# Optimization experiments

Measured on AMD Instinct MI355X. Metric: run time of the kernel, lower is better.

The kernel has to match this reference:

```python
import jax, jax.numpy as jnp
import numpy as np

K = 10  # knn neighbors
EPS = 1e-5  # BatchNorm eps


def mish(x):
    # x * tanh(softplus(x)), numerically stable softplus
    return x * jnp.tanh(jnp.logaddexp(x, 0.0))


def bn(x, g, b, m, v, nd):
    # inference-mode BatchNorm over channel axis 1
    shp = (1, -1) + (1,) * (nd - 2)
    scale = g.reshape(shp) / jnp.sqrt(v.reshape(shp) + EPS)
    return (x - m.reshape(shp)) * scale + b.reshape(shp)


def graph_feature(x, k):
    # x: [B, C, N] -> edge features [B, 2C, N, k]
    xt = jnp.swapaxes(x, 1, 2)  # [B, N, C]
    sq = jnp.sum(x * x, axis=1)  # [B, N]
    # negative squared pairwise distance [B, N, N]
    neg = 2.0 * jnp.einsum('bcn,bcm->bnm', x, x) - sq[:, :, None] - sq[:, None, :]
    idx = jax.lax.top_k(neg, k)[1]  # [B, N, k] nearest-neighbor indices
    nbr = jax.vmap(lambda a, i: a[i])(xt, idx)  # [B, N, k, C]
    ctr = jnp.broadcast_to(xt[:, :, None, :], nbr.shape)
    feat = jnp.concatenate([nbr - ctr, ctr], axis=-1)  # [B, N, k, 2C]
    return jnp.transpose(feat, (0, 3, 1, 2))  # [B, 2C, N, k]


def c2(w, x):  # 1x1 Conv2d
    return jnp.einsum('oc,bcnk->bonk', w, x)


def c1(w, x):  # 1x1 Conv1d
    return jnp.einsum('oc,bcn->bon', w, x)


def setup_inputs() -> dict:
    key = jax.random.key(0)
    ks = jax.random.split(key, 32)
    B, d, N = 8, 3, 2048
    emb, nb = 1024, 6
    def w(k_, o, c):
        return jax.random.normal(k_, (o, c), dtype=jnp.float32) * (1.0 / np.sqrt(c))
    inp = {
        'x': jax.random.normal(ks[0], (B, d, N), dtype=jnp.float32),
        'w1': w(ks[1], 64, 2 * d), 'w2': w(ks[2], 64, 64),
        'w3': w(ks[3], 64, 128), 'w4': w(ks[4], 64, 64),
        'w5': w(ks[5], 64, 128), 'w6': w(ks[6], emb, 192),
        'w7': w(ks[7], 512, emb + 192), 'w8': w(ks[8], 256, 512),
        'w9': w(ks[9], d * nb, 256),
        'g15': jax.random.uniform(ks[10], (5, 64), jnp.float32, 0.5, 1.5),
        'b15': jax.random.normal(ks[11], (5, 64), jnp.float32) * 0.1,
        'm15': jax.random.normal(ks[12], (5, 64), jnp.float32) * 0.1,
        'v15': jax.random.uniform(ks[13], (5, 64), jnp.float32, 0.5, 1.5),
        'g6': jax.random.uniform(ks[14], (emb,), jnp.float32, 0.5, 1.5),
        'b6': jax.random.normal(ks[15], (emb,), jnp.float32) * 0.1,
        'm6': jax.random.normal(ks[16], (emb,), jnp.float32) * 0.1,
        'v6': jax.random.uniform(ks[17], (emb,), jnp.float32, 0.5, 1.5),
        'g7': jax.random.uniform(ks[18], (512,), jnp.float32, 0.5, 1.5),
        'b7': jax.random.normal(ks[19], (512,), jnp.float32) * 0.1,
        'm7': jax.random.normal(ks[20], (512,), jnp.float32) * 0.1,
        'v7': jax.random.uniform(ks[21], (512,), jnp.float32, 0.5, 1.5),
        'g8': jax.random.uniform(ks[22], (256,), jnp.float32, 0.5, 1.5),
        'b8': jax.random.normal(ks[23], (256,), jnp.float32) * 0.1,
        'm8': jax.random.normal(ks[24], (256,), jnp.float32) * 0.1,
        'v8': jax.random.uniform(ks[25], (256,), jnp.float32, 0.5, 1.5),
    }
    return inp


def reference(x, w1, w2, w3, w4, w5, w6, w7, w8, w9,
              g15, b15, m15, v15, g6, b6, m6, v6,
              g7, b7, m7, v7, g8, b8, m8, v8):
    N = x.shape[2]
    f = graph_feature(x, K)                                   # [B, 6, N, K]
    h = mish(bn(c2(w1, f), g15[0], b15[0], m15[0], v15[0], 4))
    h = mish(bn(c2(w2, h), g15[1], b15[1], m15[1], v15[1], 4))
    x1 = jnp.max(h, axis=-1)                                  # [B, 64, N]
    f = graph_feature(x1, K)
    h = mish(bn(c2(w3, f), g15[2], b15[2], m15[2], v15[2], 4))
    h = mish(bn(c2(w4, h), g15[3], b15[3], m15[3], v15[3], 4))
    x2 = jnp.max(h, axis=-1)
    f = graph_feature(x2, K)
    h = mish(bn(c2(w5, f), g15[4], b15[4], m15[4], v15[4], 4))
    x3 = jnp.max(h, axis=-1)
    cat = jnp.concatenate([x1, x2, x3], axis=1)               # [B, 192, N]
    h6 = mish(bn(c1(w6, cat), g6, b6, m6, v6, 3))             # [B, emb, N]
    glob = jnp.max(h6, axis=-1, keepdims=True)
    glob = jnp.broadcast_to(glob, (glob.shape[0], glob.shape[1], N))
    h = jnp.concatenate([glob, cat], axis=1)                  # [B, emb+192, N]
    h = mish(bn(c1(w7, h), g7, b7, m7, v7, 3))
    h = mish(bn(c1(w8, h), g8, b8, m8, v8, 3))
    return c1(w9, h)                                          # [B, 18, N]
```

## Files before the change

kernel.cpp:

```cpp
#include <hip/hip_runtime.h>
#include <math.h>

#define BN_EPS 1e-5f
typedef unsigned long long u64;
typedef __attribute__((ext_vector_type(8))) short bf16x8;
typedef __attribute__((ext_vector_type(8))) unsigned short u16x8;
typedef __attribute__((ext_vector_type(4))) float f32x4;

__device__ __forceinline__ float mishf(float x){
  float u = __expf(fminf(x, 20.f));
  float w = u * (u + 2.f);
  return x * w / (w + 2.f);
}

__device__ __forceinline__ unsigned fenc(float f){
  unsigned u = __float_as_uint(f);
  return u ^ ((unsigned)((int)u >> 31) | 0x80000000u);
}
__device__ __forceinline__ float fdec(unsigned e){
  unsigned u = (e & 0x80000000u) ? (e & 0x7fffffffu) : ~e;
  return __uint_as_float(u);
}

__device__ __forceinline__ void bfsplit(float a, unsigned short &h, unsigned short &l){
  unsigned u = __float_as_uint(a);
  unsigned hb = (u + 0x7FFFu + ((u >> 16) & 1u)) >> 16;
  h = (unsigned short)hb;
  float hf = __uint_as_float(hb << 16);
  float r = a - hf;
  unsigned v = __float_as_uint(r);
  l = (unsigned short)((v + 0x7FFFu + ((v >> 16) & 1u)) >> 16);
}

__device__ __forceinline__ u64 mkkey(float v, int i){
  return ((u64)fenc(v) << 32) | (unsigned)(~i);
}
__device__ __forceinline__ int keyidx(u64 k){ return (int)(~(unsigned)k); }

__device__ __forceinline__ void ins10k(u64 (&L)[10], u64 k){
  if (k <= L[9]) return;
  #pragma unroll
  for (int p = 9; p >= 1; --p)
    L[p] = (k > L[p-1]) ? L[p-1] : ((k > L[p]) ? k : L[p]);
  L[0] = (k > L[0]) ? k : L[0];
}

__device__ __forceinline__ void ins10s(unsigned (&S)[10], unsigned e){
  #pragma unroll
  for (int p = 9; p >= 1; --p){
    unsigned ns;
    asm("v_med3_u32 %0, %1, %2, %3" : "=v"(ns) : "v"(e), "v"(S[p-1]), "v"(S[p]));
    S[p] = ns;
  }
  S[0] = (e > S[0]) ? e : S[0];
}

__device__ __forceinline__ void wavemerge10(unsigned (&S)[10], int mask){
  unsigned T[10];
  #pragma unroll
  for (int j = 0; j < 10; ++j) T[j] = __shfl_xor(S[j], mask);
  #pragma unroll
  for (int j = 0; j < 10; ++j) ins10s(S, T[j]);
}
#define KSENT mkkey(-INFINITY, 0x7fffffff)

__global__ void k_diag(float* __restrict__ out, float v){ out[0] = v; }

__global__ __launch_bounds__(256)
void k_zero(unsigned* __restrict__ p){
  p[blockIdx.x * 256 + threadIdx.x] = 0u;
}

__global__ __launch_bounds__(256)
void k_knn3(const float* __restrict__ x, int* __restrict__ idxout){
  __shared__ __align__(16) char smem[33024];
  float4* pts4   = (float4*)smem;
  unsigned* m1u  = (unsigned*)smem;
  unsigned* thr  = (unsigned*)(smem + 2560);
  int*      cnt  = (int*)(smem + 2624);
  u64*      buf  = (u64*)(smem + 2688);
  const int t  = threadIdx.x;
  const int b  = blockIdx.x >> 7;
  const int p0 = (blockIdx.x & 127) * 16;
  const int pt = t & 15, ch = t >> 4;
  const float* xb = x + (size_t)b * 6144;

  for (int i = t; i < 2048; i += 256) {
    float x0 = xb[i], x1 = xb[2048 + i], x2 = xb[4096 + i];
    float s2 = x0 * x0; s2 = fmaf(x1, x1, s2); s2 = fmaf(x2, x2, s2);
    pts4[(i >> 7) * 129 + (i & 127)] = make_float4(x0, x1, x2, s2);
  }
  __syncthreads();

  const int g = p0 + pt;
  const float4 ov = pts4[(g >> 7) * 129 + (g & 127)];
  unsigned S[10];
  #pragma unroll
  for (int j = 0; j < 10; ++j) S[j] = 0x007FFFFFu;
  const float4* cp = pts4 + ch * 129;
  #pragma unroll 4
  for (int j = 0; j < 128; ++j) {
    float4 pv = cp[j];
    float dot = ov.x * pv.x; dot = fmaf(ov.y, pv.y, dot); dot = fmaf(ov.z, pv.z, dot);
    float key = fmaf(2.f, dot, -ov.w) - pv.w;
    ins10s(S, fenc(key));
  }
  wavemerge10(S, 16);
  wavemerge10(S, 32);
  __syncthreads();

  if ((t & 48) == 0) {
    int wv = t >> 6;
    #pragma unroll
    for (int j = 0; j < 10; ++j)
      m1u[(wv * 10 + j) * 16 + pt] = S[j];
  }
  __syncthreads();

  if (t < 16) {
    unsigned F[10];
    #pragma unroll
    for (int j = 0; j < 10; ++j) F[j] = 0x007FFFFFu;
    for (int wv = 0; wv < 4; ++wv)
      #pragma unroll
      for (int j = 0; j < 10; ++j)
        ins10s(F, m1u[(wv * 10 + j) * 16 + t]);
    thr[t] = F[9];
    cnt[t] = 0;
  }
  __syncthreads();

  const unsigned th = thr[pt];
  for (int j = 0; j < 128; ++j) {
    int c = ch * 128 + j;
    float x0 = xb[c], x1 = xb[2048 + c], x2 = xb[4096 + c];
    float s2 = x0 * x0; s2 = fmaf(x1, x1, s2); s2 = fmaf(x2, x2, s2);
    float dot = ov.x * x0; dot = fmaf(ov.y, x1, dot); dot = fmaf(ov.z, x2, dot);
    float key = fmaf(2.f, dot, -ov.w) - s2;
    unsigned e = fenc(key);
    if (e >= th) {
      int slot = atomicAdd(&cnt[pt], 1);
      if (slot < 16) buf[pt * 16 + slot] = ((u64)e << 32) | (unsigned)(~c);
    }
  }
  __syncthreads();

  if (t < 16) {
    u64 F[10];
    #pragma unroll
    for (int j = 0; j < 10; ++j) F[j] = KSENT;
    int n = cnt[t]; n = (n < 16) ? n : 16;
    for (int e2 = 0; e2 < n; ++e2) ins10k(F, buf[t * 16 + e2]);
    #pragma unroll
    for (int j = 0; j < 10; ++j)
      idxout[(size_t)(b * 2048 + p0 + t) * 10 + j] = keyidx(F[j]);
  }
}

__global__ __launch_bounds__(256)
void k_knn2p(const unsigned short* __restrict__ H, const unsigned short* __restrict__ Lp,
             const float* __restrict__ sq, u64* __restrict__ pk){
  __shared__ __align__(16) char smem[9472];
  float*    ssB = (float*)smem;
  int*      cnt = (int*)(smem + 1024);
  u64*      buf = (u64*)(smem + 1280);

  const int t  = threadIdx.x;
  const int bx = blockIdx.x;
  const int cc = bx & 7;
  const int rg = (bx >> 3) & 31;
  const int b  = bx >> 8;
  const int p0 = rg * 64;
  const int c0 = cc * 256;
  const int lane = t & 63, w = t >> 6;
  const int la  = (lane & 15) * 8;
  const int sub = lane >> 4;
  const int qrow = w * 16 + (lane & 15);

  const size_t ag = ((size_t)((b * 2048 + p0) >> 4) + w) * 8 + sub;
  bf16x8 aH0 = *(const bf16x8*)&H [ ag      * 128 + la];
  bf16x8 aL0 = *(const bf16x8*)&Lp[ ag      * 128 + la];
  bf16x8 aH1 = *(const bf16x8*)&H [(ag + 4) * 128 + la];
  bf16x8 aL1 = *(const bf16x8*)&Lp[(ag + 4) * 128 + la];

  ssB[t] = sq[b * 2048 + c0 + (t & 255)];
  if (t < 64) cnt[t] = 0;
  const float nsA = -sq[b * 2048 + p0 + qrow];

  unsigned S0[10], S1[10];
  #pragma unroll
  for (int j = 0; j < 10; ++j) { S0[j] = 0x007FFFFFu; S1[j] = 0x007FFFFFu; }
  __syncthreads();

  #pragma unroll 2
  for (int m0 = 0; m0 < 256; m0 += 64) {
    const size_t cgb = ((size_t)((b * 2048 + c0 + m0) >> 4)) * 8 + sub;
    #pragma unroll
    for (int tile = 0; tile < 4; ++tile) {
      const size_t cg = (cgb + (size_t)tile * 8) * 128 + la;
      bf16x8 bH0 = *(const bf16x8*)&H [cg];
      bf16x8 bL0 = *(const bf16x8*)&Lp[cg];
      bf16x8 bH1 = *(const bf16x8*)&H [cg + 512];
      bf16x8 bL1 = *(const bf16x8*)&Lp[cg + 512];
      f32x4 acc = {0.f, 0.f, 0.f, 0.f};
      acc = __builtin_amdgcn_mfma_f32_16x16x32_bf16(bH0, aL0, acc, 0, 0, 0);
      acc = __builtin_amdgcn_mfma_f32_16x16x32_bf16(bL0, aH0, acc, 0, 0, 0);
      acc = __builtin_amdgcn_mfma_f32_16x16x32_bf16(bH0, aH0, acc, 0, 0, 0);
      acc = __builtin_amdgcn_mfma_f32_16x16x32_bf16(bH1, aL1, acc, 0, 0, 0);
      acc = __builtin_amdgcn_mfma_f32_16x16x32_bf16(bL1, aH1, acc, 0, 0, 0);
      acc = __builtin_amdgcn_mfma_f32_16x16x32_bf16(bH1, aH1, acc, 0, 0, 0);
      float4 s4 = *(const float4*)&ssB[m0 + tile * 16 + sub * 4];
      ins10s(S0, fenc(fmaf(2.f, acc[0], nsA) - s4.x));
      ins10s(S1, fenc(fmaf(2.f, acc[1], nsA) - s4.y));
      ins10s(S0, fenc(fmaf(2.f, acc[2], nsA) - s4.z));
      ins10s(S1, fenc(fmaf(2.f, acc[3], nsA) - s4.w));
    }
  }
  #pragma unroll
  for (int j = 0; j < 10; ++j) ins10s(S0, S1[j]);

  wavemerge10(S0, 16);
  wavemerge10(S0, 32);
  const unsigned thq = S0[9];

  for (int m0 = 0; m0 < 256; m0 += 64) {
    const size_t cgb = ((size_t)((b * 2048 + c0 + m0) >> 4)) * 8 + sub;
    #pragma unroll
    for (int tile = 0; tile < 4; ++tile) {
      const size_t cg = (cgb + (size_t)tile * 8) * 128 + la;
      bf16x8 bH0 = *(const bf16x8*)&H [cg];
      bf16x8 bL0 = *(const bf16x8*)&Lp[cg];
      bf16x8 bH1 = *(const bf16x8*)&H [cg + 512];
      bf16x8 bL1 = *(const bf16x8*)&Lp[cg + 512];
      f32x4 acc = {0.f, 0.f, 0.f, 0.f};
      acc = __builtin_amdgcn_mfma_f32_16x16x32_bf16(bH0, aL0, acc, 0, 0, 0);
      acc = __builtin_amdgcn_mfma_f32_16x16x32_bf16(bL0, aH0, acc, 0, 0, 0);
      acc = __builtin_amdgcn_mfma_f32_16x16x32_bf16(bH0, aH0, acc, 0, 0, 0);
      acc = __builtin_amdgcn_mfma_f32_16x16x32_bf16(bH1, aL1, acc, 0, 0, 0);
      acc = __builtin_amdgcn_mfma_f32_16x16x32_bf16(bL1, aH1, acc, 0, 0, 0);
      acc = __builtin_amdgcn_mfma_f32_16x16x32_bf16(bH1, aH1, acc, 0, 0, 0);
      float4 s4 = *(const float4*)&ssB[m0 + tile * 16 + sub * 4];
      int cbase = c0 + m0 + tile * 16 + sub * 4;
      #pragma unroll
      for (int r = 0; r < 4; ++r) {
        float sr = (r == 0) ? s4.x : (r == 1) ? s4.y : (r == 2) ? s4.z : s4.w;
        unsigned e = fenc(fmaf(2.f, acc[r], nsA) - sr);
        if (e >= thq) {
          int slot = atomicAdd(&cnt[qrow], 1);
          if (slot < 16) buf[qrow * 16 + slot] = ((u64)e << 32) | (unsigned)(~(cbase + r));
        }
      }
    }
  }
  __syncthreads();

  if (t < 64) {
    u64 F[10];
    #pragma unroll
    for (int j = 0; j < 10; ++j) F[j] = KSENT;
    int n = cnt[t]; n = (n < 16) ? n : 16;
    for (int e2 = 0; e2 < n; ++e2) ins10k(F, buf[t * 16 + e2]);
    size_t base = (size_t)(b * 2048 + p0 + t) * 80 + cc * 10;
    #pragma unroll
    for (int j = 0; j < 10; ++j) pk[base + j] = F[j];
  }
}

__global__ __launch_bounds__(64)
void k_kmerge(const u64* __restrict__ pk, int* __restrict__ idxout){
  int row = blockIdx.x * 64 + threadIdx.x;
  u64 F[10];
  #pragma unroll
  for (int j = 0; j < 10; ++j) F[j] = KSENT;
  size_t base = (size_t)row * 80;
  for (int e = 0; e < 80; ++e) ins10k(F, pk[base + e]);
  #pragma unroll
  for (int j = 0; j < 10; ++j) idxout[(size_t)row * 10 + j] = keyidx(F[j]);
}

__global__ __launch_bounds__(256)
void k_uv3(const float* __restrict__ x, const float* __restrict__ w1,
           const float* __restrict__ gg, const float* __restrict__ vv,
           float* __restrict__ UV){
  int i = blockIdx.x * 256 + threadIdx.x;
  int p = i >> 6, o = i & 63;
  int b = p >> 11, n = p & 2047;
  float s = gg[o] / sqrtf(vv[o] + BN_EPS);
  const float* xb = x + (size_t)b * 6144 + n;
  float x0 = xb[0], x1 = xb[2048], x2 = xb[4096];
  const float* wr = w1 + o * 6;
  float u = s * (wr[0] * x0 + wr[1] * x1 + wr[2] * x2);
  float v = s * ((wr[3] - wr[0]) * x0 + (wr[4] - wr[1]) * x1 + (wr[5] - wr[2]) * x2);
  UV[(size_t)p * 128 + o] = u;
  UV[(size_t)p * 128 + 64 + o] = v;
}

__global__ __launch_bounds__(256)
void k_uv(const float* __restrict__ A, int lda, int aoff,
          const float* __restrict__ w,
          const float* __restrict__ gg, const float* __restrict__ vv,
          float* __restrict__ UV){
  __shared__ float As[16][68];
  __shared__ float Bs[16][68];
  __shared__ float ss[64];
  const int t = threadIdx.x;
  const int tx = t & 15, ty = t >> 4;
  const int m0 = blockIdx.x * 64;
  const int half = blockIdx.y;
  if (t < 64) ss[t] = gg[t] / sqrtf(vv[t] + BN_EPS);
  __syncthreads();
  float acc[4][4] = {};
  for (int k0 = 0; k0 < 64; k0 += 16) {
    for (int i = t; i < 1024; i += 256) {
      int m = i >> 4, k = i & 15;
      As[k][m] = A[(size_t)(m0 + m) * lda + aoff + k0 + k];
    }
    for (int i = t; i < 1024; i += 256) {
      int n = i >> 4, k = i & 15;
      int kk = k0 + k;
      float wv = half ? (w[n * 128 + 64 + kk] - w[n * 128 + kk]) : w[n * 128 + kk];
      Bs[k][n] = wv * ss[n];
    }
    __syncthreads();
    #pragma unroll
    for (int k = 0; k < 16; ++k) {
      float4 a4 = *(const float4*)&As[k][tx * 4];
      float4 b4 = *(const float4*)&Bs[k][ty * 4];
      float am[4] = {a4.x, a4.y, a4.z, a4.w};
      float bm[4] = {b4.x, b4.y, b4.z, b4.w};
      #pragma unroll
      for (int q = 0; q < 4; ++q)
        #pragma unroll
        for (int r = 0; r < 4; ++r)
          acc[q][r] = fmaf(am[q], bm[r], acc[q][r]);
    }
    __syncthreads();
  }
  #pragma unroll
  for (int q = 0; q < 4; ++q)
    #pragma unroll
    for (int r = 0; r < 4; ++r)
      UV[(size_t)(m0 + tx * 4 + q) * 128 + half * 64 + ty * 4 + r] = acc[q][r];
}

__global__ __launch_bounds__(256)
void k_edge2(const float* __restrict__ UV, const int* __restrict__ idx,
             const float* __restrict__ w2,
             const float* __restrict__ g1, const float* __restrict__ b1,
             const float* __restrict__ m1, const float* __restrict__ v1,
             const float* __restrict__ g2, const float* __restrict__ b2,
             const float* __restrict__ m2, const float* __restrict__ v2,
             float* __restrict__ cat, int coff,
             unsigned short* __restrict__ kH, unsigned short* __restrict__ kL,
             unsigned short* __restrict__ cH, unsigned short* __restrict__ cL,
             float* __restrict__ sqout){
  __shared__ float Ha[64][81];
  __shared__ float Ws[64][68];
  __shared__ float o1s[64], s2s[64], o2s[64];
  __shared__ int   ejs[80];
  const int t = threadIdx.x;
  const int p0 = blockIdx.x * 8;
  const int batch = p0 >> 11;
  if (t < 80) ejs[t] = batch * 2048 + (idx[p0 * 10 + t] & 2047);
  if (t < 64) {
    float s1 = g1[t] / sqrtf(v1[t] + BN_EPS);
    o1s[t] = b1[t] - m1[t] * s1;
    float s2 = g2[t] / sqrtf(v2[t] + BN_EPS);
    s2s[t] = s2;
    o2s[t] = b2[t] - m2[t] * s2;
  }
  for (int i = t; i < 4096; i += 256) {
    int k = i & 63, n = i >> 6;
    Ws[k][n] = w2[n * 64 + k];
  }
  __syncthreads();

  for (int i = t; i < 5120; i += 256) {
    int e = i >> 6, c = i & 63;
    int p = p0 + e / 10;
    float hv = UV[(size_t)ejs[e] * 128 + c] + UV[(size_t)p * 128 + 64 + c] + o1s[c];
    Ha[c][e] = mishf(hv);
  }
  __syncthreads();

  const int tx = t & 15, ty = t >> 4;
  float acc[5][4] = {};
  #pragma unroll 8
  for (int k = 0; k < 64; ++k) {
    float av[5];
    #pragma unroll
    for (int i2 = 0; i2 < 5; ++i2) av[i2] = Ha[k][tx * 5 + i2];
    float4 b4 = *(const float4*)&Ws[k][ty * 4];
    float bv[4] = {b4.x, b4.y, b4.z, b4.w};
    #pragma unroll
    for (int i2 = 0; i2 < 5; ++i2)
      #pragma unroll
      for (int r = 0; r < 4; ++r)
        acc[i2][r] = fmaf(av[i2], bv[r], acc[i2][r]);
  }
  __syncthreads();
  #pragma unroll
  for (int i2 = 0; i2 < 5; ++i2)
    #pragma unroll
    for (int r = 0; r < 4; ++r) {
      int o = ty * 4 + r;
      Ha[o][tx * 5 + i2] = mishf(acc[i2][r] * s2s[o] + o2s[o]);
    }
  __syncthreads();

  for (int i = t; i < 512; i += 256) {
    int p = i >> 6, o = i & 63;
    float mx = Ha[o][p * 10];
    #pragma unroll
    for (int k = 1; k < 10; ++k) mx = fmaxf(mx, Ha[o][p * 10 + k]);
    cat[(size_t)(p0 + p) * 192 + coff + o] = mx;
    unsigned short hh, ll;
    bfsplit(mx, hh, ll);
    int n = p0 + p;
    size_t pos = ((size_t)(n >> 4) * 8 + (o >> 3)) * 128 + (n & 15) * 8 + (o & 7);
    kH[pos] = hh; kL[pos] = ll;
    int kk = coff + o;
    size_t pos192 = ((size_t)(n >> 4) * 24 + (kk >> 3)) * 128 + (n & 15) * 8 + (kk & 7);
    cH[pos192] = hh; cL[pos192] = ll;
    float r = mx * mx;
    #pragma unroll
    for (int m = 32; m; m >>= 1) r += __shfl_xor(r, m);
    if (o == 0) sqout[p0 + p] = r;
  }
}

__global__ __launch_bounds__(256)
void k_edge3(const float* __restrict__ UV, const int* __restrict__ idx,
             const float* __restrict__ gg, const float* __restrict__ bb,
             const float* __restrict__ mn, const float* __restrict__ vv,
             float* __restrict__ cat,
             unsigned short* __restrict__ cH, unsigned short* __restrict__ cL){
  int i = blockIdx.x * 256 + threadIdx.x;
  int p = i >> 6, o = i & 63;
  int batch = p >> 11;
  float s = gg[o] / sqrtf(vv[o] + BN_EPS);
  float of = bb[o] - mn[o] * s;
  float v_ = UV[(size_t)p * 128 + 64 + o] + of;
  float mx = -INFINITY;
  #pragma unroll
  for (int k = 0; k < 10; ++k) {
    int j = batch * 2048 + (idx[p * 10 + k] & 2047);
    mx = fmaxf(mx, mishf(UV[(size_t)j * 128 + o] + v_));
  }
  cat[(size_t)p * 192 + 128 + o] = mx;
  unsigned short hh, ll;
  bfsplit(mx, hh, ll);
  int kk = 128 + o;
  size_t pos192 = ((size_t)(p >> 4) * 24 + (kk >> 3)) * 128 + (p & 15) * 8 + (kk & 7);
  cH[pos192] = hh; cL[pos192] = ll;
}

__global__ __launch_bounds__(256)
void k_split(const float* __restrict__ src, int ld, int koff, int K,
             unsigned short* __restrict__ H, unsigned short* __restrict__ L){
  int i = blockIdx.x * 256 + threadIdx.x;
  int kg = K >> 3;
  int n = i / kg, g = i - n * kg;
  const float* s = &src[(size_t)n * ld + koff + g * 8];
  float4 v0 = *(const float4*)s, v1 = *(const float4*)(s + 4);
  float vv[8] = {v0.x, v0.y, v0.z, v0.w, v1.x, v1.y, v1.z, v1.w};
  u16x8 hh, ll;
  #pragma unroll
  for (int q = 0; q < 8; ++q) {
    unsigned short h_, l_;
    bfsplit(vv[q], h_, l_);
    hh[q] = h_; ll[q] = l_;
  }
  size_t pos = ((size_t)(n >> 4) * kg + g) * 128 + (n & 15) * 8;
  *(u16x8*)&H[pos] = hh;
  *(u16x8*)&L[pos] = ll;
}

#define EP_BNMISH      0
#define EP_MAXGLOB     1
#define EP_BIAS_BNMISH 2

template<int EPI>
__global__ __launch_bounds__(256)
void k_gemm(const unsigned short* __restrict__ APH, const unsigned short* __restrict__ APL,
            const unsigned short* __restrict__ WPH, const unsigned short* __restrict__ WPL,
            int K,
            const float* __restrict__ gg, const float* __restrict__ bb,
            const float* __restrict__ mn, const float* __restrict__ vv,
            const float* __restrict__ bias,
            float* __restrict__ out, int ldo,
            unsigned short* __restrict__ oH, unsigned short* __restrict__ oL, int oldo,
            unsigned* __restrict__ glob)
{
  __shared__ float red[64][17];
  const int t = threadIdx.x;
  const int lane = t & 63, w = t >> 6;
  const int m0 = blockIdx.x * 64, n0 = blockIdx.y * 64;
  const int kg = K >> 3;
  const int la = (lane & 15) * 8;
  f32x4 acc[4] = {{0,0,0,0},{0,0,0,0},{0,0,0,0},{0,0,0,0}};
  const size_t abase = ((size_t)((m0 >> 4) + w) * kg + (lane >> 4)) * 128 + la;

  for (int k0 = 0; k0 < K; k0 += 32) {
    size_t ao = abase + (size_t)(k0 >> 3) * 128;
    bf16x8 aH = *(const bf16x8*)&APH[ao];
    bf16x8 aL = *(const bf16x8*)&APL[ao];
    #pragma unroll
    for (int tt = 0; tt < 4; ++tt) {
      size_t wo = ((size_t)((n0 >> 4) + tt) * kg + (k0 >> 3) + (lane >> 4)) * 128 + la;
      bf16x8 bH = *(const bf16x8*)&WPH[wo];
      bf16x8 bL = *(const bf16x8*)&WPL[wo];
      acc[tt] = __builtin_amdgcn_mfma_f32_16x16x32_bf16(aL, bH, acc[tt], 0, 0, 0);
      acc[tt] = __builtin_amdgcn_mfma_f32_16x16x32_bf16(aH, bL, acc[tt], 0, 0, 0);
      acc[tt] = __builtin_amdgcn_mfma_f32_16x16x32_bf16(aH, bH, acc[tt], 0, 0, 0);
    }
  }

  const int mrow = m0 + w * 16 + ((lane >> 4) << 2);
  const int batch = m0 >> 11;

  if (EPI == EP_MAXGLOB) {
    #pragma unroll
    for (int tt = 0; tt < 4; ++tt) {
      int nn = n0 + tt * 16 + (lane & 15);
      float s = gg[nn] / sqrtf(vv[nn] + BN_EPS);
      float f = bb[nn] - mn[nn] * s;
      float mx = -INFINITY;
      #pragma unroll
      for (int r = 0; r < 4; ++r) mx = fmaxf(mx, mishf(acc[tt][r] * s + f));
      red[tt * 16 + (lane & 15)][w * 4 + (lane >> 4)] = mx;
    }
    __syncthreads();
    if (t < 64) {
      float v = red[t][0];
      #pragma unroll
      for (int q = 1; q < 16; ++q) v = fmaxf(v, red[t][q]);
      atomicMax(&glob[batch * 1024 + n0 + t], fenc(v));
    }
  } else {
    #pragma unroll
    for (int tt = 0; tt < 4; ++tt) {
      int nn = n0 + tt * 16 + (lane & 15);
      float s = gg[nn] / sqrtf(vv[nn] + BN_EPS);
      float f = bb[nn] - mn[nn] * s;
      float bv = (EPI == EP_BIAS_BNMISH) ? bias[batch * 512 + nn] : 0.f;
      #pragma unroll
      for (int r = 0; r < 4; ++r) {
        int m = mrow + r;
        float h = mishf((acc[tt][r] + bv) * s + f);
        if (EPI == EP_BIAS_BNMISH) {
          unsigned short hh, ll;
          bfsplit(h, hh, ll);
          size_t pos = ((size_t)(m >> 4) * (oldo >> 3) + (nn >> 3)) * 128
                       + (m & 15) * 8 + (nn & 7);
          oH[pos] = hh; oL[pos] = ll;
        } else {
          out[(size_t)m * ldo + nn] = h;
        }
      }
    }
  }
}

__global__ __launch_bounds__(64)
void k_t7(const unsigned* __restrict__ glob, const float* __restrict__ w7,
          float* __restrict__ t7){
  int bo = blockIdx.x;
  int b = bo >> 9, o = bo & 511;
  int j = threadIdx.x;
  const float* wr = w7 + (size_t)o * 1216;
  const unsigned* gr = glob + b * 1024;
  float acc = 0.f;
  #pragma unroll
  for (int c = j; c < 1024; c += 64)
    acc = fmaf(wr[c], fdec(gr[c]), acc);
  #pragma unroll
  for (int m = 32; m; m >>= 1) acc += __shfl_xor(acc, m);
  if (j == 0) t7[bo] = acc;
}

__global__ __launch_bounds__(256)
void k_out(const float* __restrict__ h8, const float* __restrict__ w9,
           float* __restrict__ out)
{
  __shared__ float row[4][256];
  const int t = threadIdx.x;
  const int g = t >> 6, l = t & 63;
  const int p = blockIdx.x * 4 + g;
  for (int c = l; c < 256; c += 64)
    row[g][c] = h8[(size_t)p * 256 + c];
  __syncthreads();
  if (l < 18) {
    float acc = 0.f;
    for (int c = 0; c < 256; ++c)
      acc = fmaf(row[g][c], w9[l * 256 + c], acc);
    int b = p >> 11, n = p & 2047;
    out[(size_t)b * 36864 + l * 2048 + n] = acc;
  }
}

extern "C" void kernel_launch(void* const* d_in, const int* in_sizes, int n_in,
                              void* d_out, int out_size, void* d_ws, size_t ws_size,
                              hipStream_t stream)
{
  const size_t OFF_IDX  = 262144;
  const size_t OFF_CAT  = 917504;
  const size_t OFF_GLOB = 13500416;
  const size_t OFF_T7   = 13533184;
  const size_t OFF_H7   = 13549568;
  const size_t OFF_KNN  = OFF_H7 + 8388608;
  const size_t OFF_PK   = OFF_H7 + 12582912;
  const size_t OFF_H8   = 47104000;
  const size_t NEED     = 63881216;

  static const int EXP[26] = {
    49152, 384, 4096, 8192, 4096, 8192, 196608, 622592, 131072, 4608,
    320, 320, 320, 320, 1024, 1024, 1024, 1024,
    512, 512, 512, 512, 256, 256, 256, 256 };
  if (n_in < 26) { k_diag<<<1,1,0,stream>>>((float*)d_out, 16384.f); return; }
  for (int i = 0; i < 26; ++i)
    if (in_sizes[i] != EXP[i]) {
      k_diag<<<1,1,0,stream>>>((float*)d_out, 4096.f + 128.f * i); return;
    }
  if (out_size != 294912) { k_diag<<<1,1,0,stream>>>((float*)d_out, 20480.f); return; }
  if (ws_size < NEED) {
    k_diag<<<1,1,0,stream>>>((float*)d_out, 24576.f + (float)(ws_size >> 20)); return;
  }

  const float* x  = (const float*)d_in[0];
  const float* w1 = (const float*)d_in[1];
  const float* w2 = (const float*)d_in[2];
  const float* w3 = (const float*)d_in[3];
  const float* w4 = (const float*)d_in[4];
  const float* w5 = (const float*)d_in[5];
  const float* w6 = (const float*)d_in[6];
  const float* w7 = (const float*)d_in[7];
  const float* w8 = (const float*)d_in[8];
  const float* w9 = (const float*)d_in[9];
  const float* g15 = (const float*)d_in[10];
  const float* b15 = (const float*)d_in[11];
  const float* m15 = (const float*)d_in[12];
  const float* v15 = (const float*)d_in[13];
  const float* g6 = (const float*)d_in[14];
  const float* b6 = (const float*)d_in[15];
  const float* m6 = (const float*)d_in[16];
  const float* v6 = (const float*)d_in[17];
  const float* g7 = (const float*)d_in[18];
  const float* b7 = (const float*)d_in[19];
  const float* m7 = (const float*)d_in[20];
  const float* v7 = (const float*)d_in[21];
  const float* g8 = (const float*)d_in[22];
  const float* b8 = (const float*)d_in[23];
  const float* m8 = (const float*)d_in[24];
  const float* v8 = (const float*)d_in[25];

  char* ws = (char*)d_ws;
  float*    sq   = (float*)(ws + 0);
  int*      idx  = (int*)(ws + OFF_IDX);
  float*    cat  = (float*)(ws + OFF_CAT);
  unsigned* glob = (unsigned*)(ws + OFF_GLOB);
  float*    t7   = (float*)(ws + OFF_T7);
  float*    UV   = (float*)(ws + OFF_H7);
  u64*      pk   = (u64*)(ws + OFF_PK);
  unsigned short* knnH = (unsigned short*)(ws + OFF_KNN);
  unsigned short* knnL = (unsigned short*)(ws + OFF_KNN + 2097152);
  float*    h8   = (float*)(ws + OFF_H8);

  unsigned short* catH = (unsigned short*)(ws + OFF_H8);
  unsigned short* catL = (unsigned short*)(ws + OFF_H8 + 6291456);
  unsigned short* h7H  = (unsigned short*)(ws + OFF_H7);
  unsigned short* h7L  = (unsigned short*)(ws + OFF_H7 + 16777216);
  unsigned short* w6H  = (unsigned short*)(ws + OFF_CAT);
  unsigned short* w6L  = (unsigned short*)(ws + OFF_CAT + 393216);
  unsigned short* w7H  = (unsigned short*)(ws + OFF_CAT + 786432);
  unsigned short* w7L  = (unsigned short*)(ws + OFF_CAT + 983040);
  unsigned short* w8H  = (unsigned short*)(ws + OFF_CAT + 1179648);
  unsigned short* w8L  = (unsigned short*)(ws + OFF_CAT + 1441792);

  k_zero<<<32, 256, 0, stream>>>(glob);

  k_knn3<<<1024, 256, 0, stream>>>(x, idx);
  k_uv3<<<4096, 256, 0, stream>>>(x, w1, g15 + 0, v15 + 0, UV);
  k_edge2<<<2048, 256, 0, stream>>>(UV, idx, w2,
      g15 + 0,  b15 + 0,  m15 + 0,  v15 + 0,
      g15 + 64, b15 + 64, m15 + 64, v15 + 64, cat, 0, knnH, knnL, catH, catL, sq);

  k_knn2p<<<2048, 256, 0, stream>>>(knnH, knnL, sq, pk);
  k_kmerge<<<256, 64, 0, stream>>>(pk, idx);
  dim3 guv(256, 2);
  k_uv<<<guv, 256, 0, stream>>>(cat, 192, 0, w3, g15 + 128, v15 + 128, UV);
  k_edge2<<<2048, 256, 0, stream>>>(UV, idx, w4,
      g15 + 128, b15 + 128, m15 + 128, v15 + 128,
      g15 + 192, b15 + 192, m15 + 192, v15 + 192, cat, 64, knnH, knnL, catH, catL, sq);

  k_knn2p<<<2048, 256, 0, stream>>>(knnH, knnL, sq, pk);
  k_kmerge<<<256, 64, 0, stream>>>(pk, idx);
  k_uv<<<guv, 256, 0, stream>>>(cat, 192, 64, w5, g15 + 256, v15 + 256, UV);
  k_edge3<<<4096, 256, 0, stream>>>(UV, idx,
      g15 + 256, b15 + 256, m15 + 256, v15 + 256, cat, catH, catL);

  k_split<<<96, 256, 0, stream>>>(w6, 192, 0, 192, w6H, w6L);
  k_split<<<48, 256, 0, stream>>>(w7, 1216, 1024, 192, w7H, w7L);
  k_split<<<64, 256, 0, stream>>>(w8, 512, 0, 512, w8H, w8L);

  dim3 g6g(256, 16);
  k_gemm<EP_MAXGLOB><<<g6g, 256, 0, stream>>>(
      catH, catL, w6H, w6L, 192, g6, b6, m6, v6,
      nullptr, nullptr, 0, nullptr, nullptr, 0, glob);
  k_t7<<<4096, 64, 0, stream>>>(glob, w7, t7);
  dim3 g7g(256, 8);
  k_gemm<EP_BIAS_BNMISH><<<g7g, 256, 0, stream>>>(
      catH, catL, w7H, w7L, 192, g7, b7, m7, v7,
      t7, nullptr, 0, h7H, h7L, 512, nullptr);
  dim3 g8g(256, 4);
  k_gemm<EP_BNMISH><<<g8g, 256, 0, stream>>>(
      h7H, h7L, w8H, w8L, 512, g8, b8, m8, v8,
      nullptr, h8, 256, nullptr, nullptr, 0, nullptr);
  k_out<<<4096, 256, 0, stream>>>(h8, w9, (float*)d_out);
}
```

Measured before the change: 587.3 us.

## Replace two-pass threshold kNN scan with single-pass index-carrying top-k

The kNN partial kernel used to compute the MFMA distance tiles twice: a first pass found a per-row threshold, and a second pass gathered the candidates above it into shared memory with atomics. It now makes one pass, keeping a register top-10 of values plus indices per lane, with an early-reject threshold test. It then merges the lanes with 64-bit shuffles. This removes half the MFMA and global loads plus the atomics, in exchange for heavier per-element insertion work (index selects) and 64-bit shuffle merges.

```diff
diff --git a/kernel.cpp b/kernel.cpp
--- a/kernel.cpp
+++ b/kernel.cpp
@@ -55,12 +55,45 @@
   S[0] = (e > S[0]) ? e : S[0];
 }
 
+#define TOPK_INIT(S, I, eth) do { \
+  _Pragma("unroll") \
+  for (int _j = 0; _j < 10; ++_j) { S[_j] = 0x007FFFFFu; I[_j] = 0x7fffffffu; } \
+  eth = 0x007FFFFFu; } while (0)
+
+__device__ __forceinline__ void topk_push32(unsigned (&S)[10], unsigned (&I)[10],
+                                            unsigned &eth, float v, unsigned i){
+  unsigned e = fenc(v);
+  if (e > eth) {
+    #pragma unroll
+    for (int p = 9; p >= 1; --p) {
+      bool gp = e > S[p-1];
+      bool gc = e > S[p];
+      I[p] = gp ? I[p-1] : (gc ? i : I[p]);
+      unsigned ns;
+      asm("v_med3_u32 %0, %1, %2, %3" : "=v"(ns) : "v"(e), "v"(S[p-1]), "v"(S[p]));
+      S[p] = ns;
+    }
+    bool g0 = e > S[0];
+    I[0] = g0 ? i : I[0];
+    S[0] = g0 ? e : S[0];
+    eth = S[9];
+  }
+}
+
 __device__ __forceinline__ void wavemerge10(unsigned (&S)[10], int mask){
   unsigned T[10];
   #pragma unroll
   for (int j = 0; j < 10; ++j) T[j] = __shfl_xor(S[j], mask);
   #pragma unroll
   for (int j = 0; j < 10; ++j) ins10s(S, T[j]);
+}
+
+__device__ __forceinline__ void wavemerge10k(u64 (&L)[10], int mask){
+  u64 T[10];
+  #pragma unroll
+  for (int j = 0; j < 10; ++j) T[j] = __shfl_xor(L[j], mask);
+  #pragma unroll
+  for (int j = 0; j < 10; ++j) ins10k(L, T[j]);
 }
 #define KSENT mkkey(-INFINITY, 0x7fffffff)
 
@@ -160,10 +193,7 @@
 __global__ __launch_bounds__(256)
 void k_knn2p(const unsigned short* __restrict__ H, const unsigned short* __restrict__ Lp,
              const float* __restrict__ sq, u64* __restrict__ pk){
-  __shared__ __align__(16) char smem[9472];
-  float*    ssB = (float*)smem;
-  int*      cnt = (int*)(smem + 1024);
-  u64*      buf = (u64*)(smem + 1280);
+  __shared__ float ssB[256];
 
   const int t  = threadIdx.x;
   const int bx = blockIdx.x;
@@ -184,44 +214,11 @@
   bf16x8 aL1 = *(const bf16x8*)&Lp[(ag + 4) * 128 + la];
 
   ssB[t] = sq[b * 2048 + c0 + (t & 255)];
-  if (t < 64) cnt[t] = 0;
   const float nsA = -sq[b * 2048 + p0 + qrow];
 
-  unsigned S0[10], S1[10];
-  #pragma unroll
-  for (int j = 0; j < 10; ++j) { S0[j] = 0x007FFFFFu; S1[j] = 0x007FFFFFu; }
-  __syncthreads();
-
-  #pragma unroll 2
-  for (int m0 = 0; m0 < 256; m0 += 64) {
-    const size_t cgb = ((size_t)((b * 2048 + c0 + m0) >> 4)) * 8 + sub;
-    #pragma unroll
-    for (int tile = 0; tile < 4; ++tile) {
-      const size_t cg = (cgb + (size_t)tile * 8) * 128 + la;
-      bf16x8 bH0 = *(const bf16x8*)&H [cg];
-      bf16x8 bL0 = *(const bf16x8*)&Lp[cg];
-      bf16x8 bH1 = *(const bf16x8*)&H [cg + 512];
-      bf16x8 bL1 = *(const bf16x8*)&Lp[cg + 512];
-      f32x4 acc = {0.f, 0.f, 0.f, 0.f};
-      acc = __builtin_amdgcn_mfma_f32_16x16x32_bf16(bH0, aL0, acc, 0, 0, 0);
-      acc = __builtin_amdgcn_mfma_f32_16x16x32_bf16(bL0, aH0, acc, 0, 0, 0);
-      acc = __builtin_amdgcn_mfma_f32_16x16x32_bf16(bH0, aH0, acc, 0, 0, 0);
-      acc = __builtin_amdgcn_mfma_f32_16x16x32_bf16(bH1, aL1, acc, 0, 0, 0);
-      acc = __builtin_amdgcn_mfma_f32_16x16x32_bf16(bL1, aH1, acc, 0, 0, 0);
-      acc = __builtin_amdgcn_mfma_f32_16x16x32_bf16(bH1, aH1, acc, 0, 0, 0);
-      float4 s4 = *(const float4*)&ssB[m0 + tile * 16 + sub * 4];
-      ins10s(S0, fenc(fmaf(2.f, acc[0], nsA) - s4.x));
-      ins10s(S1, fenc(fmaf(2.f, acc[1], nsA) - s4.y));
-      ins10s(S0, fenc(fmaf(2.f, acc[2], nsA) - s4.z));
-      ins10s(S1, fenc(fmaf(2.f, acc[3], nsA) - s4.w));
-    }
-  }
-  #pragma unroll
-  for (int j = 0; j < 10; ++j) ins10s(S0, S1[j]);
-
-  wavemerge10(S0, 16);
-  wavemerge10(S0, 32);
-  const unsigned thq = S0[9];
+  unsigned S[10], I[10], eth;
+  TOPK_INIT(S, I, eth);
+  __syncthreads();
 
   for (int m0 = 0; m0 < 256; m0 += 64) {
     const size_t cgb = ((size_t)((b * 2048 + c0 + m0) >> 4)) * 8 + sub;
@@ -241,28 +238,24 @@
       acc = __builtin_amdgcn_mfma_f32_16x16x32_bf16(bH1, aH1, acc, 0, 0, 0);
       float4 s4 = *(const float4*)&ssB[m0 + tile * 16 + sub * 4];
       int cbase = c0 + m0 + tile * 16 + sub * 4;
-      #pragma unroll
-      for (int r = 0; r < 4; ++r) {
-        float sr = (r == 0) ? s4.x : (r == 1) ? s4.y : (r == 2) ? s4.z : s4.w;
-        unsigned e = fenc(fmaf(2.f, acc[r], nsA) - sr);
-        if (e >= thq) {
-          int slot = atomicAdd(&cnt[qrow], 1);
-          if (slot < 16) buf[qrow * 16 + slot] = ((u64)e << 32) | (unsigned)(~(cbase + r));
-        }
-      }
-    }
-  }
-  __syncthreads();
-
-  if (t < 64) {
-    u64 F[10];
-    #pragma unroll
-    for (int j = 0; j < 10; ++j) F[j] = KSENT;
-    int n = cnt[t]; n = (n < 16) ? n : 16;
-    for (int e2 = 0; e2 < n; ++e2) ins10k(F, buf[t * 16 + e2]);
-    size_t base = (size_t)(b * 2048 + p0 + t) * 80 + cc * 10;
-    #pragma unroll
-    for (int j = 0; j < 10; ++j) pk[base + j] = F[j];
+      topk_push32(S, I, eth, fmaf(2.f, acc[0], nsA) - s4.x, cbase);
+      topk_push32(S, I, eth, fmaf(2.f, acc[1], nsA) - s4.y, cbase + 1);
+      topk_push32(S, I, eth, fmaf(2.f, acc[2], nsA) - s4.z, cbase + 2);
+      topk_push32(S, I, eth, fmaf(2.f, acc[3], nsA) - s4.w, cbase + 3);
+    }
+  }
+
+  u64 L[10];
+  #pragma unroll
+  for (int j = 0; j < 10; ++j)
+    L[j] = ((u64)S[j] << 32) | (unsigned)(~I[j]);
+  wavemerge10k(L, 16);
+  wavemerge10k(L, 32);
+
+  if (sub == 0) {
+    size_t base = (size_t)(b * 2048 + p0 + qrow) * 80 + cc * 10;
+    #pragma unroll
+    for (int j = 0; j < 10; ++j) pk[base + j] = L[j];
   }
 }
 
```

Result: slower. 623.1 us (+6.1%).
